# Kernel optimization log

Hardware: AMD Instinct MI355X
Metric: run time of the kernel (lower is better)

The kernel has to match this reference:

```python
import jax, jax.numpy as jnp
import numpy as np

E = 32                       # early_it: number of leading K-dims used for the stats test
BOUND = -2.053748910631823   # norm.ppf(0.02)


def setup_inputs() -> dict:
    key = jax.random.key(0)
    k1, k2, k3 = jax.random.split(key, 3)
    B, S, H, OUT = 2, 2048, 2048, 8192
    x = jax.random.normal(k1, (B, S, H), dtype=jnp.float32)
    weight = jax.random.normal(k2, (OUT, H), dtype=jnp.float32) * (1.0 / np.sqrt(H))
    bias = jax.random.normal(k3, (OUT,), dtype=jnp.float32) * 0.02
    stats_w = jnp.ones((), dtype=jnp.float32)
    stats_b = jnp.zeros((), dtype=jnp.float32)
    return {"x": x, "weight": weight, "bias": bias, "stats_w": stats_w, "stats_b": stats_b}


def reference(x, weight, bias, stats_w, stats_b):
    B, S, H = x.shape
    OUT = weight.shape[0]
    x2 = x.reshape(B * S, H)           # [N, H]
    x_e, x_t = x2[:, :E], x2[:, E:]    # [N, E], [N, H-E]
    w_e, w_t = weight[:, :E], weight[:, E:]

    # partial GEMM over the first E dims + running sum of squares
    y1 = x_e @ w_e.T + bias[None, :]                 # [N, OUT]
    cum_sq = (x_e * x_e) @ (w_e * w_e).T             # [N, OUT]

    # exact stats test (torch_stats_test_ref_exact)
    n = jnp.float32(E)
    cur_mean = (y1 / n) * stats_w + stats_b
    cur_var = (cum_sq / n - cur_mean * cur_mean) * stats_w * stats_w
    test_stats = cur_mean / jnp.sqrt(cur_var / n)
    passed = test_stats < BOUND                      # [N, OUT] bool

    # remaining partial GEMM, then masked combine
    y2 = x_t @ w_t.T
    y = jnp.where(passed, jnp.zeros_like(y1), y1 + y2)
    return y.reshape(B, S, OUT)
```

## Files before the change

### kernel.cpp

```cpp
#include <hip/hip_runtime.h>
#include <hip/hip_bf16.h>
#include <hip/hip_fp16.h>
#include <stdint.h>

#define M_DIM 4096
#define K_DIM 2048
#define N_DIM 8192

typedef __attribute__((ext_vector_type(4))) float f32x4;
typedef __attribute__((ext_vector_type(8))) _Float16 f16x8;

typedef __attribute__((address_space(1))) const unsigned int g_u32_t;
typedef __attribute__((address_space(3))) unsigned int lds_u32_t;

static __device__ __forceinline__ void gload16(const void* g, void* l) {
  __builtin_amdgcn_global_load_lds((g_u32_t*)g, (lds_u32_t*)l, 16, 0, 0);
}

#define BOUNDF ((float)(-2.053748910631823))

__device__ __forceinline__ unsigned char gate_passed(float y1v, float sqv,
                                                     float sw, float sb) {
  float cm = y1v / 32.0f * sw + sb;
  float cv = (sqv / 32.0f - cm * cm) * sw * sw;
  float ts = cm / sqrtf(cv / 32.0f);
  return (ts < BOUNDF) ? (unsigned char)1 : (unsigned char)0;
}

__global__ void cvt_f16_fused_kernel(const float* __restrict__ x,
                                     const float* __restrict__ wgt,
                                     unsigned short* __restrict__ xf,
                                     unsigned short* __restrict__ wf,
                                     float* __restrict__ xe,
                                     float* __restrict__ we,
                                     int n4x, int n4tot) {
  int i = blockIdx.x * blockDim.x + threadIdx.x;
  int stride = gridDim.x * blockDim.x;
  for (; i < n4tot; i += stride) {
    const float* src;
    unsigned short* dst;
    float* pe;
    int idx;
    if (i < n4x) {
      src = x; dst = xf; pe = xe; idx = i;
    } else {
      src = wgt; dst = wf; pe = we; idx = i - n4x;
    }
    float4 v = reinterpret_cast<const float4*>(src)[idx];
    int col4 = idx & (K_DIM / 4 - 1);
    if (col4 < 8) {
      int row = idx >> 9;
      reinterpret_cast<float4*>(pe)[row * 8 + col4] = v;
    }
    float xs[4] = {v.x, v.y, v.z, v.w};
    unsigned short hb[4];
#pragma unroll
    for (int j = 0; j < 4; ++j) {
      _Float16 h = (_Float16)xs[j];
      hb[j] = *reinterpret_cast<unsigned short*>(&h);
    }
    reinterpret_cast<ushort4*>(dst)[idx] = make_ushort4(hb[0], hb[1], hb[2], hb[3]);
  }
}

__global__ __launch_bounds__(256, 2) void gemm_f16_kernel(
    const unsigned short* __restrict__ xf, const unsigned short* __restrict__ wf,
    const float* __restrict__ xe_packed, const float* __restrict__ we_packed,
    const float* __restrict__ bias, const float* __restrict__ swp,
    const float* __restrict__ sbp, float* __restrict__ out) {
  __shared__ __align__(16) unsigned char smem_bytes[128 * 32 * 4 + 32 * 128 * 4];
  unsigned short* smem = (unsigned short*)smem_bytes;

  int bid = blockIdx.x;
  int sid = (bid & 7) * 256 + (bid >> 3);
  int bm = sid >> 6;
  int bn = sid & 63;
  int row0 = bm * 128, col0 = bn * 128;

  int t = threadIdx.x, lane = t & 63, w = t >> 6;
  int wrow = (w >> 1) * 64, wcol = (w & 1) * 64;

  int Lr[2], Lg[2];
#pragma unroll
  for (int i = 0; i < 2; ++i) {
    int L = (w * 2 + i) * 1024 + lane * 16;
    int row = L >> 6;
    int s = (L >> 4) & 3;
    Lr[i] = row;
    Lg[i] = s ^ ((row >> 1) & 3);
  }

  int aoff[4], boff[4];
  int g = lane >> 4;
#pragma unroll
  for (int m = 0; m < 4; ++m) {
    int row = wrow + m * 16 + (lane & 15);
    aoff[m] = row * 32 + ((g ^ ((row >> 1) & 3)) * 8);
  }
#pragma unroll
  for (int n = 0; n < 4; ++n) {
    int row = wcol + n * 16 + (lane & 15);
    boff[n] = row * 32 + ((g ^ ((row >> 1) & 3)) * 8);
  }

  f32x4 acc[4][4];
#pragma unroll
  for (int m = 0; m < 4; ++m)
#pragma unroll
    for (int n = 0; n < 4; ++n) acc[m][n] = (f32x4){0.0f, 0.0f, 0.0f, 0.0f};

  const unsigned short* gpa0 = xf + (size_t)(row0 + Lr[0]) * K_DIM + Lg[0] * 8;
  const unsigned short* gpa1 = xf + (size_t)(row0 + Lr[1]) * K_DIM + Lg[1] * 8;
  const unsigned short* gpb0 = wf + (size_t)(col0 + Lr[0]) * K_DIM + Lg[0] * 8;
  const unsigned short* gpb1 = wf + (size_t)(col0 + Lr[1]) * K_DIM + Lg[1] * 8;
  char* lpa0 = (char*)smem + (w * 2 + 0) * 1024;
  char* lpa1 = (char*)smem + (w * 2 + 1) * 1024;
  char* lpb0 = lpa0 + 8192;
  char* lpb1 = lpa1 + 8192;

#pragma unroll 1
  for (int kt = 0; kt < K_DIM / 32; ++kt) {
    gload16(gpa0, lpa0);
    gload16(gpa1, lpa1);
    gload16(gpb0, lpb0);
    gload16(gpb1, lpb1);
    gpa0 += 32; gpa1 += 32; gpb0 += 32; gpb1 += 32;
    __syncthreads();

    f16x8 a[4], b[4];
#pragma unroll
    for (int m = 0; m < 4; ++m)
      a[m] = *reinterpret_cast<const f16x8*>(&smem[0 * 4096 + aoff[m]]);
#pragma unroll
    for (int n = 0; n < 4; ++n)
      b[n] = *reinterpret_cast<const f16x8*>(&smem[1 * 4096 + boff[n]]);
#pragma unroll
    for (int m = 0; m < 4; ++m)
#pragma unroll
      for (int n = 0; n < 4; ++n)
        acc[m][n] = __builtin_amdgcn_mfma_f32_16x16x32_f16(a[m], b[n], acc[m][n], 0, 0, 0);
    __syncthreads();
  }

  float* xe_lds = (float*)smem_bytes;
  float* we_lds = (float*)(smem_bytes + 128 * 32 * 4);

#pragma unroll
  for (int it = 0; it < 4; ++it) {
    int idx = it * 256 + t;
    int r = idx >> 3, q = idx & 7;
    float4 v = reinterpret_cast<const float4*>(xe_packed)[(size_t)(row0 + r) * 8 + q];
    *reinterpret_cast<float4*>(&xe_lds[r * 32 + q * 4]) = v;
  }
#pragma unroll
  for (int it = 0; it < 4; ++it) {
    int idx = it * 256 + t;
    int c = idx & 127, kq = idx >> 7;
    float4 v = reinterpret_cast<const float4*>(we_packed)[(size_t)(col0 + c) * 8 + kq];
    we_lds[(kq * 4 + 0) * 128 + c] = v.x;
    we_lds[(kq * 4 + 1) * 128 + c] = v.y;
    we_lds[(kq * 4 + 2) * 128 + c] = v.z;
    we_lds[(kq * 4 + 3) * 128 + c] = v.w;
  }
  __syncthreads();

  float sw = *swp, sb = *sbp;
  int cl = lane & 15, rg = lane >> 4;

#pragma unroll
  for (int m = 0; m < 4; ++m) {
    float y1[4][4], sq[4][4];
#pragma unroll
    for (int j = 0; j < 4; ++j)
#pragma unroll
      for (int n = 0; n < 4; ++n) { y1[j][n] = 0.0f; sq[j][n] = 0.0f; }
    int rb0 = wrow + m * 16 + rg * 4;
#pragma unroll 4
    for (int k = 0; k < 32; ++k) {
      float wv[4], wv2[4];
#pragma unroll
      for (int n = 0; n < 4; ++n) {
        wv[n] = we_lds[k * 128 + wcol + n * 16 + cl];
        wv2[n] = wv[n] * wv[n];
      }
#pragma unroll
      for (int j = 0; j < 4; ++j) {
        float xv = xe_lds[(rb0 + j) * 32 + k];
        float xv2 = xv * xv;
#pragma unroll
        for (int n = 0; n < 4; ++n) {
          y1[j][n] = fmaf(xv, wv[n], y1[j][n]);
          sq[j][n] = fmaf(xv2, wv2[n], sq[j][n]);
        }
      }
    }
#pragma unroll
    for (int n = 0; n < 4; ++n) {
      int c = col0 + wcol + n * 16 + cl;
      float bv = bias[c];
#pragma unroll
      for (int j = 0; j < 4; ++j) {
        float v = acc[m][n][j] + bv;
        float y1v = y1[j][n] + bv;
        unsigned char p = gate_passed(y1v, sq[j][n], sw, sb);
        int r = row0 + wrow + m * 16 + rg * 4 + j;
        out[(size_t)r * N_DIM + c] = p ? 0.0f : v;
      }
    }
  }
}

__device__ __forceinline__ void stats4x4(const float* __restrict__ x,
                                         const float* __restrict__ w,
                                         int r0, int c0,
                                         float (&y1)[4][4], float (&sq)[4][4]) {
#pragma unroll
  for (int i = 0; i < 4; ++i)
#pragma unroll
    for (int j = 0; j < 4; ++j) { y1[i][j] = 0.0f; sq[i][j] = 0.0f; }
#pragma unroll
  for (int kc = 0; kc < 8; ++kc) {
    float4 xa[4], wa[4], x2[4], w2[4];
#pragma unroll
    for (int i = 0; i < 4; ++i)
      xa[i] = *reinterpret_cast<const float4*>(x + (size_t)(r0 + i) * K_DIM + kc * 4);
#pragma unroll
    for (int j = 0; j < 4; ++j)
      wa[j] = *reinterpret_cast<const float4*>(w + (size_t)(c0 + j) * K_DIM + kc * 4);
#pragma unroll
    for (int i = 0; i < 4; ++i)
      x2[i] = make_float4(xa[i].x * xa[i].x, xa[i].y * xa[i].y,
                          xa[i].z * xa[i].z, xa[i].w * xa[i].w);
#pragma unroll
    for (int j = 0; j < 4; ++j)
      w2[j] = make_float4(wa[j].x * wa[j].x, wa[j].y * wa[j].y,
                          wa[j].z * wa[j].z, wa[j].w * wa[j].w);
#pragma unroll
    for (int i = 0; i < 4; ++i)
#pragma unroll
      for (int j = 0; j < 4; ++j) {
        float a = y1[i][j];
        a = fmaf(xa[i].x, wa[j].x, a);
        a = fmaf(xa[i].y, wa[j].y, a);
        a = fmaf(xa[i].z, wa[j].z, a);
        a = fmaf(xa[i].w, wa[j].w, a);
        y1[i][j] = a;
        float b = sq[i][j];
        b = fmaf(x2[i].x, w2[j].x, b);
        b = fmaf(x2[i].y, w2[j].y, b);
        b = fmaf(x2[i].z, w2[j].z, b);
        b = fmaf(x2[i].w, w2[j].w, b);
        sq[i][j] = b;
      }
  }
}

__global__ void fallback_gemm_kernel(const float* __restrict__ x, const float* __restrict__ wgt,
                                     const float* __restrict__ bias, const float* __restrict__ swp,
                                     const float* __restrict__ sbp, float* __restrict__ out) {
  __shared__ float xs[64][36], ws2[64][36];
  int t = threadIdx.x;
  int tr = t >> 4, tc = t & 15;
  int r0 = blockIdx.x * 64, c0 = blockIdx.y * 64;
  float acc[4][4];
#pragma unroll
  for (int i = 0; i < 4; ++i)
#pragma unroll
    for (int j = 0; j < 4; ++j) acc[i][j] = 0.0f;

#pragma unroll 1
  for (int kt = 0; kt < K_DIM / 32; ++kt) {
#pragma unroll
    for (int i = 0; i < 2; ++i) {
      int idx = t + 256 * i;
      int row = idx >> 3;
      int kk = (idx & 7) * 4;
      *reinterpret_cast<float4*>(&xs[row][kk]) =
          *reinterpret_cast<const float4*>(x + (size_t)(r0 + row) * K_DIM + kt * 32 + kk);
      *reinterpret_cast<float4*>(&ws2[row][kk]) =
          *reinterpret_cast<const float4*>(wgt + (size_t)(c0 + row) * K_DIM + kt * 32 + kk);
    }
    __syncthreads();
#pragma unroll 4
    for (int k = 0; k < 32; ++k) {
      float xv[4], wv[4];
#pragma unroll
      for (int i = 0; i < 4; ++i) { xv[i] = xs[tr * 4 + i][k]; wv[i] = ws2[tc * 4 + i][k]; }
#pragma unroll
      for (int i = 0; i < 4; ++i)
#pragma unroll
        for (int j = 0; j < 4; ++j) acc[i][j] = fmaf(xv[i], wv[j], acc[i][j]);
    }
    __syncthreads();
  }

  float y1[4][4], sq[4][4];
  stats4x4(x, wgt, r0 + tr * 4, c0 + tc * 4, y1, sq);
  float sw = *swp, sb = *sbp;
#pragma unroll
  for (int i = 0; i < 4; ++i)
#pragma unroll
    for (int j = 0; j < 4; ++j) {
      int r = r0 + tr * 4 + i, c = c0 + tc * 4 + j;
      float bv = bias[c];
      unsigned char p = gate_passed(y1[i][j] + bv, sq[i][j], sw, sb);
      out[(size_t)r * N_DIM + c] = p ? 0.0f : (acc[i][j] + bv);
    }
}

extern "C" void kernel_launch(void* const* d_in, const int* in_sizes, int n_in,
                              void* d_out, int out_size, void* d_ws, size_t ws_size,
                              hipStream_t stream) {
  (void)in_sizes; (void)n_in; (void)out_size;
  const float* x    = (const float*)d_in[0];
  const float* wgt  = (const float*)d_in[1];
  const float* bias = (const float*)d_in[2];
  const float* swp  = (const float*)d_in[3];
  const float* sbp  = (const float*)d_in[4];
  float* out = (float*)d_out;

  const size_t xf_off = 0;
  const size_t wf_off = xf_off + (size_t)M_DIM * K_DIM * 2;
  const size_t xe_off = wf_off + (size_t)N_DIM * K_DIM * 2;
  const size_t we_off = xe_off + (size_t)M_DIM * 32 * 4;
  const size_t need   = we_off + (size_t)N_DIM * 32 * 4;

  if (ws_size >= need) {
    unsigned short* xf = (unsigned short*)((char*)d_ws + xf_off);
    unsigned short* wf = (unsigned short*)((char*)d_ws + wf_off);
    float* xe = (float*)((char*)d_ws + xe_off);
    float* we = (float*)((char*)d_ws + we_off);

    int n4x = M_DIM * K_DIM / 4;
    int n4tot = n4x + N_DIM * K_DIM / 4;
    hipLaunchKernelGGL(cvt_f16_fused_kernel, dim3(2048), dim3(256), 0, stream,
                       x, wgt, xf, wf, xe, we, n4x, n4tot);
    hipLaunchKernelGGL(gemm_f16_kernel, dim3(2048), dim3(256), 0, stream,
                       xf, wf, xe, we, bias, swp, sbp, out);
  } else {
    hipLaunchKernelGGL(fallback_gemm_kernel, dim3(M_DIM / 64, N_DIM / 64), dim3(256), 0, stream,
                       x, wgt, bias, swp, sbp, out);
  }
}
```

Before: 292.4 us.

## Split stats-test gating into separate mask kernel, GEMM epilogue reads byte mask

Moves the fp32 early-dims stats computation out of the GEMM epilogue into a dedicated mask kernel that writes a per-element byte mask to workspace. The GEMM epilogue now only reads the mask and applies the bias and zeroing, which shrinks its LDS use and register pressure. The mask kernel pads the xe LDS rows to stride 36 to avoid bank conflicts. An asm barrier on cm*cm stops the compiler from contracting it into an FMA, keeping the gate arithmetic matching the reference. The cost is an extra launch plus writing and reading a 32 MB mask.

Result: slower. 315.7 us (+8.0%).

```diff
diff --git a/kernel.cpp b/kernel.cpp
--- a/kernel.cpp
+++ b/kernel.cpp
@@ -22,7 +22,9 @@
 __device__ __forceinline__ unsigned char gate_passed(float y1v, float sqv,
                                                      float sw, float sb) {
   float cm = y1v / 32.0f * sw + sb;
-  float cv = (sqv / 32.0f - cm * cm) * sw * sw;
+  float cmsq = cm * cm;
+  asm volatile("" : "+v"(cmsq));
+  float cv = (sqv / 32.0f - cmsq) * sw * sw;
   float ts = cm / sqrtf(cv / 32.0f);
   return (ts < BOUNDF) ? (unsigned char)1 : (unsigned char)0;
 }
@@ -63,13 +65,85 @@
   }
 }
 
+__global__ __launch_bounds__(256, 2) void mask_kernel(
+    const float* __restrict__ xe_packed, const float* __restrict__ we_packed,
+    const float* __restrict__ bias, const float* __restrict__ swp,
+    const float* __restrict__ sbp, unsigned char* __restrict__ mask) {
+  __shared__ __align__(16) unsigned char smem_bytes[128 * 36 * 4 + 32 * 128 * 4];
+  float* xe_lds = (float*)smem_bytes;
+  float* we_lds = (float*)(smem_bytes + 128 * 36 * 4);
+
+  int row0 = blockIdx.x * 128, col0 = blockIdx.y * 128;
+  int t = threadIdx.x, lane = t & 63, w = t >> 6;
+  int wrow = (w >> 1) * 64, wcol = (w & 1) * 64;
+  int cl = lane & 15, rg = lane >> 4;
+
+#pragma unroll
+  for (int it = 0; it < 4; ++it) {
+    int idx = it * 256 + t;
+    int r = idx >> 3, q = idx & 7;
+    float4 v = reinterpret_cast<const float4*>(xe_packed)[(size_t)(row0 + r) * 8 + q];
+    *reinterpret_cast<float4*>(&xe_lds[r * 36 + q * 4]) = v;
+  }
+#pragma unroll
+  for (int it = 0; it < 4; ++it) {
+    int idx = it * 256 + t;
+    int c = idx & 127, kq = idx >> 7;
+    float4 v = reinterpret_cast<const float4*>(we_packed)[(size_t)(col0 + c) * 8 + kq];
+    we_lds[(kq * 4 + 0) * 128 + c] = v.x;
+    we_lds[(kq * 4 + 1) * 128 + c] = v.y;
+    we_lds[(kq * 4 + 2) * 128 + c] = v.z;
+    we_lds[(kq * 4 + 3) * 128 + c] = v.w;
+  }
+  __syncthreads();
+
+  float sw = *swp, sb = *sbp;
+
+#pragma unroll
+  for (int m = 0; m < 4; ++m) {
+    float y1[4][4], sq[4][4];
+#pragma unroll
+    for (int j = 0; j < 4; ++j)
+#pragma unroll
+      for (int n = 0; n < 4; ++n) { y1[j][n] = 0.0f; sq[j][n] = 0.0f; }
+    int rb0 = wrow + m * 16 + rg * 4;
+#pragma unroll 4
+    for (int k = 0; k < 32; ++k) {
+      float wv[4], wv2[4];
+#pragma unroll
+      for (int n = 0; n < 4; ++n) {
+        wv[n] = we_lds[k * 128 + wcol + n * 16 + cl];
+        wv2[n] = wv[n] * wv[n];
+      }
+#pragma unroll
+      for (int j = 0; j < 4; ++j) {
+        float xv = xe_lds[(rb0 + j) * 36 + k];
+        float xv2 = xv * xv;
+#pragma unroll
+        for (int n = 0; n < 4; ++n) {
+          y1[j][n] = fmaf(xv, wv[n], y1[j][n]);
+          sq[j][n] = fmaf(xv2, wv2[n], sq[j][n]);
+        }
+      }
+    }
+#pragma unroll
+    for (int n = 0; n < 4; ++n) {
+      int c = col0 + wcol + n * 16 + cl;
+      float bv = bias[c];
+#pragma unroll
+      for (int j = 0; j < 4; ++j) {
+        int r = row0 + rb0 + j;
+        mask[(size_t)r * N_DIM + c] = gate_passed(y1[j][n] + bv, sq[j][n], sw, sb);
+      }
+    }
+  }
+}
+
 __global__ __launch_bounds__(256, 2) void gemm_f16_kernel(
     const unsigned short* __restrict__ xf, const unsigned short* __restrict__ wf,
-    const float* __restrict__ xe_packed, const float* __restrict__ we_packed,
-    const float* __restrict__ bias, const float* __restrict__ swp,
-    const float* __restrict__ sbp, float* __restrict__ out) {
-  __shared__ __align__(16) unsigned char smem_bytes[128 * 32 * 4 + 32 * 128 * 4];
-  unsigned short* smem = (unsigned short*)smem_bytes;
+    const float* __restrict__ bias, const unsigned char* __restrict__ mask,
+    float* __restrict__ out) {
+  __shared__ __align__(16) unsigned short smem[2 * 4096];
 
   int bid = blockIdx.x;
   int sid = (bid & 7) * 256 + (bid >> 3);
@@ -142,69 +216,18 @@
     __syncthreads();
   }
 
-  float* xe_lds = (float*)smem_bytes;
-  float* we_lds = (float*)(smem_bytes + 128 * 32 * 4);
-
-#pragma unroll
-  for (int it = 0; it < 4; ++it) {
-    int idx = it * 256 + t;
-    int r = idx >> 3, q = idx & 7;
-    float4 v = reinterpret_cast<const float4*>(xe_packed)[(size_t)(row0 + r) * 8 + q];
-    *reinterpret_cast<float4*>(&xe_lds[r * 32 + q * 4]) = v;
-  }
-#pragma unroll
-  for (int it = 0; it < 4; ++it) {
-    int idx = it * 256 + t;
-    int c = idx & 127, kq = idx >> 7;
-    float4 v = reinterpret_cast<const float4*>(we_packed)[(size_t)(col0 + c) * 8 + kq];
-    we_lds[(kq * 4 + 0) * 128 + c] = v.x;
-    we_lds[(kq * 4 + 1) * 128 + c] = v.y;
-    we_lds[(kq * 4 + 2) * 128 + c] = v.z;
-    we_lds[(kq * 4 + 3) * 128 + c] = v.w;
-  }
-  __syncthreads();
-
-  float sw = *swp, sb = *sbp;
   int cl = lane & 15, rg = lane >> 4;
-
 #pragma unroll
   for (int m = 0; m < 4; ++m) {
-    float y1[4][4], sq[4][4];
-#pragma unroll
-    for (int j = 0; j < 4; ++j)
-#pragma unroll
-      for (int n = 0; n < 4; ++n) { y1[j][n] = 0.0f; sq[j][n] = 0.0f; }
-    int rb0 = wrow + m * 16 + rg * 4;
-#pragma unroll 4
-    for (int k = 0; k < 32; ++k) {
-      float wv[4], wv2[4];
-#pragma unroll
-      for (int n = 0; n < 4; ++n) {
-        wv[n] = we_lds[k * 128 + wcol + n * 16 + cl];
-        wv2[n] = wv[n] * wv[n];
-      }
-#pragma unroll
-      for (int j = 0; j < 4; ++j) {
-        float xv = xe_lds[(rb0 + j) * 32 + k];
-        float xv2 = xv * xv;
-#pragma unroll
-        for (int n = 0; n < 4; ++n) {
-          y1[j][n] = fmaf(xv, wv[n], y1[j][n]);
-          sq[j][n] = fmaf(xv2, wv2[n], sq[j][n]);
-        }
-      }
-    }
+    int rb = row0 + wrow + m * 16 + rg * 4;
 #pragma unroll
     for (int n = 0; n < 4; ++n) {
       int c = col0 + wcol + n * 16 + cl;
       float bv = bias[c];
 #pragma unroll
       for (int j = 0; j < 4; ++j) {
-        float v = acc[m][n][j] + bv;
-        float y1v = y1[j][n] + bv;
-        unsigned char p = gate_passed(y1v, sq[j][n], sw, sb);
-        int r = row0 + wrow + m * 16 + rg * 4 + j;
-        out[(size_t)r * N_DIM + c] = p ? 0.0f : v;
+        size_t idx = (size_t)(rb + j) * N_DIM + c;
+        out[idx] = mask[idx] ? 0.0f : (acc[m][n][j] + bv);
       }
     }
   }
@@ -323,20 +346,24 @@
   const size_t wf_off = xf_off + (size_t)M_DIM * K_DIM * 2;
   const size_t xe_off = wf_off + (size_t)N_DIM * K_DIM * 2;
   const size_t we_off = xe_off + (size_t)M_DIM * 32 * 4;
-  const size_t need   = we_off + (size_t)N_DIM * 32 * 4;
+  const size_t mk_off = we_off + (size_t)N_DIM * 32 * 4;
+  const size_t need   = mk_off + (size_t)M_DIM * N_DIM;
 
   if (ws_size >= need) {
     unsigned short* xf = (unsigned short*)((char*)d_ws + xf_off);
     unsigned short* wf = (unsigned short*)((char*)d_ws + wf_off);
     float* xe = (float*)((char*)d_ws + xe_off);
     float* we = (float*)((char*)d_ws + we_off);
+    unsigned char* mk  = (unsigned char*)((char*)d_ws + mk_off);
 
     int n4x = M_DIM * K_DIM / 4;
     int n4tot = n4x + N_DIM * K_DIM / 4;
     hipLaunchKernelGGL(cvt_f16_fused_kernel, dim3(2048), dim3(256), 0, stream,
                        x, wgt, xf, wf, xe, we, n4x, n4tot);
+    hipLaunchKernelGGL(mask_kernel, dim3(M_DIM / 128, N_DIM / 128), dim3(256), 0, stream,
+                       xe, we, bias, swp, sbp, mk);
     hipLaunchKernelGGL(gemm_f16_kernel, dim3(2048), dim3(256), 0, stream,
-                       xf, wf, xe, we, bias, swp, sbp, out);
+                       xf, wf, bias, mk, out);
   } else {
     hipLaunchKernelGGL(fallback_gemm_kernel, dim3(M_DIM / 64, N_DIM / 64), dim3(256), 0, stream,
                        x, wgt, bias, swp, sbp, out);
```
